# Performance work log

Hardware: AMD Instinct MI355X
Metric: run time of the kernel (lower is better)

## Reference

```python
import jax, jax.numpy as jnp
import numpy as np

B, J, V, G, D = 1, 24, 20000, 2, 3
DCIN = J * 12          # num_parts * (9 + 3)
DC = 4                 # d_cond
HID = 128
BETA = 100.0           # softplus beta
EPS = 1e-8


def softplus_b(x):
    return jax.nn.softplus(BETA * x) / BETA


def group_linear(x, W, b):
    # x: (J, N, din), W: (J, din, dout), b: (J, dout)
    return jnp.einsum('jnd,jdo->jno', x, W) + b[:, None, :]


def axis_angle_to_matrix(aa):
    # aa: (..., 3) -> (..., 3, 3), Rodrigues formula
    angle = jnp.linalg.norm(aa, axis=-1, keepdims=True)
    axis = aa / jnp.where(angle < 1e-12, 1.0, angle)
    x, y, z = axis[..., 0], axis[..., 1], axis[..., 2]
    a = angle[..., 0]
    c, s = jnp.cos(a), jnp.sin(a)
    C = 1.0 - c
    r0 = jnp.stack([c + x * x * C, x * y * C - z * s, x * z * C + y * s], axis=-1)
    r1 = jnp.stack([y * x * C + z * s, c + y * y * C, y * z * C - x * s], axis=-1)
    r2 = jnp.stack([z * x * C - y * s, z * y * C + x * s, c + z * z * C], axis=-1)
    return jnp.stack([r0, r1, r2], axis=-2)


def blending_weights(pts, Jtr_center, Jtr_neigh, Jtr_self, bid_this, bid_other, rigid_alpha, rigid_beta):
    # pts: (B,J,V,3); Jtr_*: (B,J,1,3); bid_*: (J,) int
    ra = jax.nn.elu(rigid_alpha - 1.0) + 1.0
    a_n = ra[bid_other, bid_this].reshape(1, -1, 1, 1)
    a_s = ra[bid_this, bid_other].reshape(1, -1, 1, 1)
    be_n = rigid_beta[bid_other, bid_this].reshape(1, -1, 1, 1)
    be_s = rigid_beta[bid_this, bid_other].reshape(1, -1, 1, 1)
    vec_bone_n = Jtr_neigh - Jtr_center
    vec_bone_s = Jtr_self - Jtr_center
    nb_n = jnp.linalg.norm(vec_bone_n, axis=-1, keepdims=True)
    nb_s = jnp.linalg.norm(vec_bone_s, axis=-1, keepdims=True)
    vb_n = (Jtr_neigh - Jtr_self) / (nb_n + nb_s + EPS) * nb_n
    vb_s = -vb_n / (nb_n + EPS) * nb_s
    n_n = jnp.linalg.norm(vb_n, axis=-1, keepdims=True)
    n_s = jnp.linalg.norm(vb_s, axis=-1, keepdims=True)
    tr_o = Jtr_neigh - vb_n
    vec_pts = jax.lax.stop_gradient(pts) - tr_o   # pts.detach() in torch
    d_n = vb_n / (n_n + EPS)
    d_s = vb_s / (n_s + EPS)
    r_n = jnp.sum(vec_pts * d_n, axis=-1, keepdims=True) / (n_n + EPS)
    r_s = jnp.sum(vec_pts * d_s, axis=-1, keepdims=True) / (n_s + EPS)
    return jax.nn.sigmoid((r_n * a_n + be_n) - (r_s * a_s + be_s))


def _forward(pts, Bcond, Btr, Brot, Bneigh, rigid_alpha, rigid_beta,
             cW0, cb0, cW1, cb1, cW2, cb2, W0, b0, W1, b1, W2, b2, W3, b3):
    # world -> per-part local coords: (B,J,V,3)
    Brot_inv = jnp.swapaxes(Brot, -1, -2)
    pts_local = jnp.einsum('bjxy,bjvy->bjvx', Brot_inv, pts[:, None] - Btr[:, :, None])
    # neighbor-based deformation offsets
    ids = jax.lax.stop_gradient(Bneigh[0, :, :, 4, :2]).astype(jnp.int32)  # (J,G,2)
    offset_sum = jnp.zeros_like(pts_local)
    for gi in range(G):  # small fixed neighbor count
        Jtr_this = Bneigh[:, :, gi, 0][:, :, None]    # (B,J,1,3)
        Jtr_center = Bneigh[:, :, gi, 1][:, :, None]
        Jtr_other = Bneigh[:, :, gi, 2][:, :, None]
        Jpose = Bneigh[:, :, gi, 3][:, :, None]
        w = blending_weights(pts_local, Jtr_center, Jtr_other, Jtr_this,
                             ids[:, gi, 0], ids[:, gi, 1], rigid_alpha, rigid_beta)  # (B,J,V,1)
        Jp_w = jnp.nan_to_num(Jpose * w)              # (B,J,V,3)
        R = axis_angle_to_matrix(-Jp_w)               # (B,J,V,3,3)
        off = jnp.einsum('bjvxy,bjvy->bjvx', R, pts_local - Jtr_center) + Jtr_center - pts_local
        offset_sum = offset_sum + jnp.nan_to_num(off)
    pts_local = pts_local + offset_sum
    # grouped per-part MLP (INR with num_groups=J)
    x_in = jnp.transpose(pts_local, (1, 0, 2, 3)).reshape(J, B * V, D)
    cond = jnp.broadcast_to(jnp.transpose(Bcond, (1, 0, 2))[:, :, None, :], (J, B, V, DCIN)).reshape(J, B * V, DCIN)
    c = softplus_b(group_linear(cond, cW0, cb0))
    c = softplus_b(group_linear(c, cW1, cb1))
    c = group_linear(c, cW2, cb2)                      # (J, BV, 4)
    x = jnp.concatenate([x_in, c], axis=-1)            # (J, BV, 7)
    x = softplus_b(group_linear(x, W0, b0))
    x = softplus_b(group_linear(x, W1, b1))
    x = softplus_b(group_linear(x, W2, b2))
    x = group_linear(x, W3, b3)                        # (J, BV, 1)
    pred_parts = jnp.transpose(x.reshape(J, B, V, 1), (1, 0, 2, 3))  # (B,J,V,1)
    # softmin blend over parts
    pred_min = jnp.min(pred_parts, axis=1)             # (B,V,1)
    delta = pred_parts - pred_min[:, None]
    wsm = jax.nn.softmax(-delta * 200.0, axis=1)       # Softmin(dim=1)
    return jnp.sum(delta * wsm, axis=1) + pred_min


def setup_inputs() -> dict:
    key = jax.random.key(0)
    ks = jax.random.split(key, 16)
    pts = jax.random.normal(ks[0], (B, V, D), jnp.float32)
    Bcond = jax.random.normal(ks[1], (B, J, DCIN), jnp.float32) * 0.1
    Btr = jax.random.normal(ks[2], (B, J, D), jnp.float32)
    Brot = jax.random.normal(ks[3], (B, J, D, D), jnp.float32)
    core = jax.random.normal(ks[4], (B, J, G, 4, D), jnp.float32) * 0.5
    ids_this = jnp.arange(J, dtype=jnp.float32)
    ids_o0 = jnp.mod(jnp.arange(J) + 1, J).astype(jnp.float32)
    ids_o1 = jnp.mod(jnp.arange(J) - 1, J).astype(jnp.float32)
    bid = jnp.zeros((B, J, G, 1, D), jnp.float32)
    bid = bid.at[:, :, 0, 0, 0].set(ids_this).at[:, :, 0, 0, 1].set(ids_o0)
    bid = bid.at[:, :, 1, 0, 0].set(ids_this).at[:, :, 1, 0, 1].set(ids_o1)
    Bneigh = jnp.concatenate([core, bid], axis=-2)     # (B,J,G,5,D)
    rigid_alpha = jnp.full((J, J), 2.0, jnp.float32)   # blend_alpha init
    rigid_beta = jnp.zeros((J, J), jnp.float32)
    def gl(k, din, dout, std):
        return jax.random.normal(k, (J, din, dout), jnp.float32) * std, jnp.zeros((J, dout), jnp.float32)
    cW0, cb0 = gl(ks[5], DCIN, DC * 4, float(np.sqrt(2.0 / DCIN)))
    cW1, cb1 = gl(ks[6], DC * 4, DC * 4, float(np.sqrt(2.0 / (DC * 4))))
    cW2, cb2 = gl(ks[7], DC * 4, DC, 1e-5)
    std_h = float(np.sqrt(2.0) / np.sqrt(HID))
    W0, b0 = gl(ks[8], D + DC, HID, std_h)
    W1, b1 = gl(ks[9], HID, HID, std_h)
    W2, b2 = gl(ks[10], HID, HID, std_h)
    W3 = jax.random.normal(ks[11], (J, HID, 1), jnp.float32) * 1e-5 + float(np.sqrt(np.pi) / np.sqrt(HID))
    b3 = jnp.full((J, 1), -1.0, jnp.float32)           # -radius_init
    return {'pts': pts, 'Bcond': Bcond, 'Btr': Btr, 'Brot': Brot, 'Bneigh': Bneigh,
            'rigid_alpha': rigid_alpha, 'rigid_beta': rigid_beta,
            'cW0': cW0, 'cb0': cb0, 'cW1': cW1, 'cb1': cb1, 'cW2': cW2, 'cb2': cb2,
            'W0': W0, 'b0': b0, 'W1': W1, 'b1': b1, 'W2': W2, 'b2': b2, 'W3': W3, 'b3': b3}


def reference(pts, Bcond, Btr, Brot, Bneigh, rigid_alpha, rigid_beta,
              cW0, cb0, cW1, cb1, cW2, cb2, W0, b0, W1, b1, W2, b2, W3, b3):
    return _forward(pts, Bcond, Btr, Brot, Bneigh, rigid_alpha, rigid_beta,
                    cW0, cb0, cW1, cb1, cW2, cb2, W0, b0, W1, b1, W2, b2, W3, b3)
```

## Files before the change

kernel.cpp:

```cpp
#include <hip/hip_runtime.h>
#include <hip/hip_bf16.h>
#include <math.h>

#define VN 20000
#define JN 24
#define TILE 64
#define KP 132
#define EPSF 1e-8f

typedef __attribute__((ext_vector_type(8))) short bfrag;
typedef __attribute__((ext_vector_type(4))) float f32x4;

#define WJ_STRIDE 139264
#define L0A 0
#define L0B 4096
#define L1A 8192
#define L1B 40960
#define L2A 73728
#define L2B 106496

__device__ __forceinline__ unsigned short f2bf(float x) {
    __hip_bfloat16 b = __float2bfloat16(x);
    unsigned short u; __builtin_memcpy(&u, &b, 2); return u;
}
__device__ __forceinline__ float bf2f(unsigned short u) {
    __hip_bfloat16 b; __builtin_memcpy(&b, &u, 2);
    return __bfloat162float(b);
}
__device__ __forceinline__ unsigned int pack_hl(float x) {
    const unsigned int h = (__float_as_uint(x) + 0x8000u) & 0xffff0000u;
    const float hf = __uint_as_float(h);
    const float lo = x - hf;
    unsigned int r;
    asm("v_cvt_pk_bf16_f32 %0, %1, %2" : "=v"(r) : "v"(hf), "v"(lo));
    return r;
}

__device__ __forceinline__ float softplus_fast(float x) {
    const float u = __builtin_amdgcn_exp2f(-144.269504f * fabsf(x));
    float p = fmaf(u, 3.04480e-4f, -1.31584e-3f);
    p = fmaf(u, p, 2.852768e-3f);
    p = fmaf(u, p, -4.902308e-3f);
    p = fmaf(u, p, 9.992342e-3f);
    p = fmaf(u, p, 8.0e-8f);
    return fmaxf(x, 0.0f) + p;
}

__global__ __launch_bounds__(384) void prep_kernel(
    const float* __restrict__ Bcond, const float* __restrict__ Bneigh,
    const float* __restrict__ ralpha, const float* __restrict__ rbeta,
    const float* __restrict__ cW0, const float* __restrict__ cb0,
    const float* __restrict__ cW1, const float* __restrict__ cb1,
    const float* __restrict__ cW2, const float* __restrict__ cb2,
    float* __restrict__ c4, float* __restrict__ geom)
{
    __shared__ float hbuf[JN][16];
    const int t = threadIdx.x;

    if (t < JN * 2) {
        const int j = t >> 1, gi = t & 1;
        const float* nb = Bneigh + (j * 2 + gi) * 15;
        const float tx = nb[0],  ty = nb[1],  tz = nb[2];
        const float cx = nb[3],  cy = nb[4],  cz = nb[5];
        const float ox = nb[6],  oy = nb[7],  oz = nb[8];
        const float px = nb[9],  py = nb[10], pz = nb[11];
        const int bid_this  = (int)nb[12];
        const int bid_other = (int)nb[13];
        const float xa_n = ralpha[bid_other * JN + bid_this] - 1.0f;
        const float xa_s = ralpha[bid_this * JN + bid_other] - 1.0f;
        const float a_n = xa_n > 0.0f ? xa_n + 1.0f : expf(xa_n);
        const float a_s = xa_s > 0.0f ? xa_s + 1.0f : expf(xa_s);
        const float be_n = rbeta[bid_other * JN + bid_this];
        const float be_s = rbeta[bid_this * JN + bid_other];

        const float bnx = ox - cx, bny = oy - cy, bnz = oz - cz;
        const float bsx = tx - cx, bsy = ty - cy, bsz = tz - cz;
        const float nb_n = sqrtf(bnx*bnx + bny*bny + bnz*bnz);
        const float nb_s = sqrtf(bsx*bsx + bsy*bsy + bsz*bsz);
        const float f = nb_n / (nb_n + nb_s + EPSF);
        const float vbnx = (ox - tx) * f, vbny = (oy - ty) * f, vbnz = (oz - tz) * f;
        const float g2 = -nb_s / (nb_n + EPSF);
        const float vbsx = vbnx * g2, vbsy = vbny * g2, vbsz = vbnz * g2;
        const float n_n = sqrtf(vbnx*vbnx + vbny*vbny + vbnz*vbnz);
        const float n_s = sqrtf(vbsx*vbsx + vbsy*vbsy + vbsz*vbsz);
        const float trx = ox - vbnx, tr_y = oy - vbny, trz = oz - vbnz;
        const float inn = 1.0f / ((n_n + EPSF) * (n_n + EPSF));
        const float ins = 1.0f / ((n_s + EPSF) * (n_s + EPSF));
        const float gx = vbnx * inn * a_n - vbsx * ins * a_s;
        const float gy = vbny * inn * a_n - vbsy * ins * a_s;
        const float gz = vbnz * inn * a_n - vbsz * ins * a_s;
        const float h = -(trx * gx + tr_y * gy + trz * gz) + be_n - be_s;
        float* gm = geom + (j * 2 + gi) * 12;
        gm[0] = gx; gm[1] = gy; gm[2] = gz; gm[3] = h;
        gm[4] = px; gm[5] = py; gm[6] = pz;
        gm[7] = cx; gm[8] = cy; gm[9] = cz;
        gm[10] = 0.0f; gm[11] = 0.0f;
    }

    {
        const int j = t >> 4, o = t & 15;
        const float* cond = Bcond + j * 288;
        const float* w = cW0 + j * 288 * 16 + o;
        float acc = cb0[j * 16 + o];
        for (int d = 0; d < 288; ++d) acc = fmaf(cond[d], w[d * 16], acc);
        hbuf[j][o] = softplus_fast(acc);
    }
    __syncthreads();
    {
        const int j = t >> 4, o = t & 15;
        const float* w = cW1 + j * 256 + o;
        float acc = cb1[j * 16 + o];
        #pragma unroll
        for (int d = 0; d < 16; ++d) acc = fmaf(hbuf[j][d], w[d * 16], acc);
        acc = softplus_fast(acc);
        __syncthreads();
        hbuf[j][o] = acc;
    }
    __syncthreads();
    if (t < JN * 4) {
        const int j = t >> 2, o = t & 3;
        const float* w = cW2 + j * 64 + o;
        float acc = cb2[j * 4 + o];
        #pragma unroll
        for (int d = 0; d < 16; ++d) acc = fmaf(hbuf[j][d], w[d * 4], acc);
        c4[j * 4 + o] = acc;
    }
}

__global__ __launch_bounds__(256) void wprep_kernel(
    const float* __restrict__ W0, const float* __restrict__ W1,
    const float* __restrict__ W2, unsigned short* __restrict__ wt)
{
    const int g = blockIdx.x * 256 + threadIdx.x;
    const int jj = g / 17408;
    const int r = (g - jj * 17408) * 8;
    const float* src; int kin, pr; bool loP;
    if (r < 8192)       { src = W0 + jj * 896;   kin = 7;   pr = r & 4095;          loP = r >= L0B; }
    else if (r < 73728) { src = W1 + jj * 16384; kin = 128; pr = (r - L1A) & 32767; loP = r >= L1B; }
    else                { src = W2 + jj * 16384; kin = 128; pr = (r - L2A) & 32767; loP = r >= L2B; }
    const int lane = (pr >> 3) & 63;
    const int nt   = (pr >> 9) & 7;
    const int ks   = pr >> 12;
    const int n  = nt * 16 + (lane & 15);
    const int k0 = (ks * 32 + (lane >> 4) * 8) >> 1;
    unsigned short out[8];
    #pragma unroll
    for (int kk = 0; kk < 4; ++kk) {
        const float v = (k0 + kk < kin) ? src[(k0 + kk) * 128 + n] : 0.0f;
        const unsigned short h = f2bf(v);
        if (!loP) { out[2*kk] = h; out[2*kk+1] = h; }
        else      { out[2*kk] = f2bf(v - bf2f(h)); out[2*kk+1] = 0; }
    }
    *(uint4*)(wt + jj * WJ_STRIDE + r) = *(const uint4*)out;
}

template<int NKS>
__device__ __forceinline__ void mfma_layer(
    unsigned int* __restrict__ X,
    const unsigned short* __restrict__ wA,
    const unsigned short* __restrict__ wB,
    const float* __restrict__ bvec,
    int q, int lane)
{
    const int l = lane & 15;
    const int quad = lane >> 4;
    const float bia0 = bvec[q * 32 + l];
    const float bia1 = bvec[q * 32 + 16 + l];
    f32x4 acc[4][2];
    #pragma unroll
    for (int mi = 0; mi < 4; ++mi) {
        acc[mi][0] = (f32x4){bia0, bia0, bia0, bia0};
        acc[mi][1] = (f32x4){bia1, bia1, bia1, bia1};
    }

    #pragma unroll 2
    for (int ks = 0; ks < NKS; ++ks) {
        bfrag bA[2], bB[2];
        #pragma unroll
        for (int ni = 0; ni < 2; ++ni) {
            const int off = ((ks * 8 + (q * 2 + ni)) * 64 + lane) * 8;
            bA[ni] = *(const bfrag*)(wA + off);
            bB[ni] = *(const bfrag*)(wB + off);
        }
        #pragma unroll
        for (int mi = 0; mi < 4; ++mi) {
            const bfrag a = *(const bfrag*)(
                (const unsigned short*)(X + (mi * 16 + l) * KP) + ks * 32 + quad * 8);
            #pragma unroll
            for (int ni = 0; ni < 2; ++ni) {
                acc[mi][ni] = __builtin_amdgcn_mfma_f32_16x16x32_bf16(a, bA[ni], acc[mi][ni], 0, 0, 0);
                acc[mi][ni] = __builtin_amdgcn_mfma_f32_16x16x32_bf16(a, bB[ni], acc[mi][ni], 0, 0, 0);
            }
        }
    }
    __syncthreads();
    #pragma unroll
    for (int ni = 0; ni < 2; ++ni) {
        const int ch = q * 32 + ni * 16 + l;
        #pragma unroll
        for (int mi = 0; mi < 4; ++mi) {
            #pragma unroll
            for (int r = 0; r < 4; ++r) {
                const float v = softplus_fast(acc[mi][ni][r]);
                const int p = mi * 16 + quad * 4 + r;
                X[p * KP + ch] = pack_hl(v);
            }
        }
    }
    __syncthreads();
}

__global__ __launch_bounds__(256, 4) void main_kernel(
    const float* __restrict__ pts, const float* __restrict__ Btr,
    const float* __restrict__ Brot,
    const float* __restrict__ b0, const float* __restrict__ b1,
    const float* __restrict__ b2, const float* __restrict__ W3,
    const float* __restrict__ b3,
    const float* __restrict__ c4, const float* __restrict__ geom,
    const unsigned short* __restrict__ wt,
    float* __restrict__ pred)
{
    __shared__ unsigned int X[TILE * KP];
    const int j = blockIdx.y;
    const int v0 = blockIdx.x * TILE;
    const int t = threadIdx.x;
    const int lane = t & 63;
    const int q = __builtin_amdgcn_readfirstlane(t >> 6);

    if (t < TILE) {
        const int v = v0 + t;
        float plx = 0.0f, ply = 0.0f, plz = 0.0f;
        if (v < VN) {
            const float dx = pts[v * 3 + 0] - Btr[j * 3 + 0];
            const float dy = pts[v * 3 + 1] - Btr[j * 3 + 1];
            const float dz = pts[v * 3 + 2] - Btr[j * 3 + 2];
            const float* R = Brot + j * 9;
            plx = R[0] * dx + R[3] * dy + R[6] * dz;
            ply = R[1] * dx + R[4] * dy + R[7] * dz;
            plz = R[2] * dx + R[5] * dy + R[8] * dz;
            float osx = 0.0f, osy = 0.0f, osz = 0.0f;
            #pragma unroll
            for (int gi = 0; gi < 2; ++gi) {
                const float* gm = geom + (j * 2 + gi) * 12;
                const float arg = plx * gm[0] + ply * gm[1] + plz * gm[2] + gm[3];
                const float w = 1.0f / (1.0f + __expf(-arg));
                const float aax = -gm[4] * w, aay = -gm[5] * w, aaz = -gm[6] * w;
                const float jcx = gm[7], jcy = gm[8], jcz = gm[9];
                const float ang = sqrtf(aax * aax + aay * aay + aaz * aaz);
                const float inv = ang < 1e-12f ? 1.0f : 1.0f / ang;
                const float ux = aax * inv, uy = aay * inv, uz = aaz * inv;
                const float co = __cosf(ang), si = __sinf(ang), C = 1.0f - co;
                const float vx = plx - jcx, vy = ply - jcy, vz = plz - jcz;
                const float du = ux * vx + uy * vy + uz * vz;
                const float cxv = uy * vz - uz * vy;
                const float cyv = uz * vx - ux * vz;
                const float czv = ux * vy - uy * vx;
                float offx = co * vx + si * cxv + C * ux * du + jcx - plx;
                float offy = co * vy + si * cyv + C * uy * du + jcy - ply;
                float offz = co * vz + si * czv + C * uz * du + jcz - plz;
                if (isnan(offx)) offx = 0.0f;
                if (isnan(offy)) offy = 0.0f;
                if (isnan(offz)) offz = 0.0f;
                osx += offx; osy += offy; osz += offz;
            }
            plx += osx; ply += osy; plz += osz;
        }
        X[t * KP + 0] = pack_hl(plx);
        X[t * KP + 1] = pack_hl(ply);
        X[t * KP + 2] = pack_hl(plz);
        X[t * KP + 3] = pack_hl(c4[j * 4 + 0]);
        X[t * KP + 4] = pack_hl(c4[j * 4 + 1]);
        X[t * KP + 5] = pack_hl(c4[j * 4 + 2]);
        X[t * KP + 6] = pack_hl(c4[j * 4 + 3]);
        #pragma unroll
        for (int k = 7; k < 16; ++k) X[t * KP + k] = 0u;
    }
    __syncthreads();

    const unsigned short* wj = wt + j * WJ_STRIDE;
    mfma_layer<1>(X, wj + L0A, wj + L0B, b0 + j * 128, q, lane);
    mfma_layer<8>(X, wj + L1A, wj + L1B, b1 + j * 128, q, lane);
    mfma_layer<8>(X, wj + L2A, wj + L2B, b2 + j * 128, q, lane);

    {
        const float* w3 = W3 + j * 128 + q * 32;
        float part = 0.0f;
        #pragma unroll 8
        for (int kk = 0; kk < 32; ++kk) {
            const unsigned int d = X[lane * KP + q * 32 + kk];
            const float xv = __uint_as_float(d << 16)
                           + __uint_as_float(d & 0xffff0000u);
            part = fmaf(xv, w3[kk], part);
        }
        X[lane * KP + 128 + q] = __float_as_uint(part);
    }
    __syncthreads();
    if (t < TILE) {
        const int v = v0 + t;
        const float r = b3[j]
            + __uint_as_float(X[t * KP + 128]) + __uint_as_float(X[t * KP + 129])
            + __uint_as_float(X[t * KP + 130]) + __uint_as_float(X[t * KP + 131]);
        if (v < VN) pred[j * VN + v] = r;
    }
}

__global__ __launch_bounds__(256) void softmin_kernel(const float* __restrict__ pred,
                                                      float* __restrict__ out)
{
    const int v = blockIdx.x * 256 + threadIdx.x;
    if (v >= VN) return;
    float vals[JN];
    float m = 3.4e38f;
    #pragma unroll
    for (int jj = 0; jj < JN; ++jj) {
        vals[jj] = pred[jj * VN + v];
        m = fminf(m, vals[jj]);
    }
    float s1 = 0.0f, s2 = 0.0f;
    #pragma unroll
    for (int jj = 0; jj < JN; ++jj) {
        const float d = vals[jj] - m;
        const float e = __expf(-200.0f * d);
        s1 += e;
        s2 = fmaf(d, e, s2);
    }
    out[v] = s2 / s1 + m;
}

extern "C" void kernel_launch(void* const* d_in, const int* in_sizes, int n_in,
                              void* d_out, int out_size, void* d_ws, size_t ws_size,
                              hipStream_t stream)
{
    const float* pts    = (const float*)d_in[0];
    const float* Bcond  = (const float*)d_in[1];
    const float* Btr    = (const float*)d_in[2];
    const float* Brot   = (const float*)d_in[3];
    const float* Bneigh = (const float*)d_in[4];
    const float* ralpha = (const float*)d_in[5];
    const float* rbeta  = (const float*)d_in[6];
    const float* cW0 = (const float*)d_in[7];
    const float* cb0 = (const float*)d_in[8];
    const float* cW1 = (const float*)d_in[9];
    const float* cb1 = (const float*)d_in[10];
    const float* cW2 = (const float*)d_in[11];
    const float* cb2 = (const float*)d_in[12];
    const float* W0 = (const float*)d_in[13];
    const float* b0 = (const float*)d_in[14];
    const float* W1 = (const float*)d_in[15];
    const float* b1 = (const float*)d_in[16];
    const float* W2 = (const float*)d_in[17];
    const float* b2 = (const float*)d_in[18];
    const float* W3 = (const float*)d_in[19];
    const float* b3 = (const float*)d_in[20];

    float* ws   = (float*)d_ws;
    float* pred = ws;
    float* c4   = ws + JN * VN;
    float* geom = c4 + JN * 4;
    unsigned short* wt = (unsigned short*)(geom + JN * 2 * 12);

    prep_kernel<<<1, 384, 0, stream>>>(Bcond, Bneigh, ralpha, rbeta,
                                       cW0, cb0, cW1, cb1, cW2, cb2, c4, geom);

    wprep_kernel<<<(JN * 17408) / 256, 256, 0, stream>>>(W0, W1, W2, wt);

    dim3 grid((VN + TILE - 1) / TILE, JN);
    main_kernel<<<grid, 256, 0, stream>>>(pts, Btr, Brot,
                                          b0, b1, b2, W3, b3,
                                          c4, geom, wt, pred);

    softmin_kernel<<<(VN + 255) / 256, 256, 0, stream>>>(pred, (float*)d_out);
}
```

Measured before the change: 262.2 us.

## Merge prep kernels and remap main grid so each XCD owns three parts

```diff
diff --git a/kernel.cpp b/kernel.cpp
--- a/kernel.cpp
+++ b/kernel.cpp
@@ -7,6 +7,8 @@
 #define TILE 64
 #define KP 132
 #define EPSF 1e-8f
+#define NXB 313
+#define WPREP_BLOCKS 1632
 
 typedef __attribute__((ext_vector_type(8))) short bfrag;
 typedef __attribute__((ext_vector_type(4))) float f32x4;
@@ -46,7 +48,9 @@
     return fmaxf(x, 0.0f) + p;
 }
 
-__global__ __launch_bounds__(384) void prep_kernel(
+__global__ __launch_bounds__(256) void setup_kernel(
+    const float* __restrict__ W0, const float* __restrict__ W1,
+    const float* __restrict__ W2, unsigned short* __restrict__ wt,
     const float* __restrict__ Bcond, const float* __restrict__ Bneigh,
     const float* __restrict__ ralpha, const float* __restrict__ rbeta,
     const float* __restrict__ cW0, const float* __restrict__ cb0,
@@ -54,11 +58,41 @@
     const float* __restrict__ cW2, const float* __restrict__ cb2,
     float* __restrict__ c4, float* __restrict__ geom)
 {
-    __shared__ float hbuf[JN][16];
+    if (blockIdx.x < WPREP_BLOCKS) {
+        const int g = blockIdx.x * 256 + threadIdx.x;
+        const int jj = g / 17408;
+        const int r = (g - jj * 17408) * 8;
+        const float* src; int kin, pr; bool loP;
+        if (r < 8192)       { src = W0 + jj * 896;   kin = 7;   pr = r & 4095;          loP = r >= L0B; }
+        else if (r < 73728) { src = W1 + jj * 16384; kin = 128; pr = (r - L1A) & 32767; loP = r >= L1B; }
+        else                { src = W2 + jj * 16384; kin = 128; pr = (r - L2A) & 32767; loP = r >= L2B; }
+        const int lane = (pr >> 3) & 63;
+        const int nt   = (pr >> 9) & 7;
+        const int ks   = pr >> 12;
+        const int n  = nt * 16 + (lane & 15);
+        const int k0 = (ks * 32 + (lane >> 4) * 8) >> 1;
+        unsigned short out[8];
+        #pragma unroll
+        for (int kk = 0; kk < 4; ++kk) {
+            const float v = (k0 + kk < kin) ? src[(k0 + kk) * 128 + n] : 0.0f;
+            const unsigned short h = f2bf(v);
+            if (!loP) { out[2*kk] = h; out[2*kk+1] = h; }
+            else      { out[2*kk] = f2bf(v - bf2f(h)); out[2*kk+1] = 0; }
+        }
+        *(uint4*)(wt + jj * WJ_STRIDE + r) = *(const uint4*)out;
+        return;
+    }
+
+    __shared__ float cond_s[288];
+    __shared__ float sh[16][17];
+    __shared__ float hb[16];
+    const int j = blockIdx.x - WPREP_BLOCKS;
     const int t = threadIdx.x;
 
-    if (t < JN * 2) {
-        const int j = t >> 1, gi = t & 1;
+    for (int i = t; i < 288; i += 256) cond_s[i] = Bcond[j * 288 + i];
+
+    if (t < 2) {
+        const int gi = t;
         const float* nb = Bneigh + (j * 2 + gi) * 15;
         const float tx = nb[0],  ty = nb[1],  tz = nb[2];
         const float cx = nb[3],  cy = nb[4],  cz = nb[5];
@@ -96,62 +130,40 @@
         gm[7] = cx; gm[8] = cy; gm[9] = cz;
         gm[10] = 0.0f; gm[11] = 0.0f;
     }
+    __syncthreads();
 
     {
-        const int j = t >> 4, o = t & 15;
-        const float* cond = Bcond + j * 288;
+        const int o = t & 15, c = t >> 4;
         const float* w = cW0 + j * 288 * 16 + o;
-        float acc = cb0[j * 16 + o];
-        for (int d = 0; d < 288; ++d) acc = fmaf(cond[d], w[d * 16], acc);
-        hbuf[j][o] = softplus_fast(acc);
-    }
-    __syncthreads();
-    {
-        const int j = t >> 4, o = t & 15;
-        const float* w = cW1 + j * 256 + o;
-        float acc = cb1[j * 16 + o];
-        #pragma unroll
-        for (int d = 0; d < 16; ++d) acc = fmaf(hbuf[j][d], w[d * 16], acc);
-        acc = softplus_fast(acc);
-        __syncthreads();
-        hbuf[j][o] = acc;
-    }
-    __syncthreads();
-    if (t < JN * 4) {
-        const int j = t >> 2, o = t & 3;
-        const float* w = cW2 + j * 64 + o;
-        float acc = cb2[j * 4 + o];
-        #pragma unroll
-        for (int d = 0; d < 16; ++d) acc = fmaf(hbuf[j][d], w[d * 4], acc);
-        c4[j * 4 + o] = acc;
-    }
-}
-
-__global__ __launch_bounds__(256) void wprep_kernel(
-    const float* __restrict__ W0, const float* __restrict__ W1,
-    const float* __restrict__ W2, unsigned short* __restrict__ wt)
-{
-    const int g = blockIdx.x * 256 + threadIdx.x;
-    const int jj = g / 17408;
-    const int r = (g - jj * 17408) * 8;
-    const float* src; int kin, pr; bool loP;
-    if (r < 8192)       { src = W0 + jj * 896;   kin = 7;   pr = r & 4095;          loP = r >= L0B; }
-    else if (r < 73728) { src = W1 + jj * 16384; kin = 128; pr = (r - L1A) & 32767; loP = r >= L1B; }
-    else                { src = W2 + jj * 16384; kin = 128; pr = (r - L2A) & 32767; loP = r >= L2B; }
-    const int lane = (pr >> 3) & 63;
-    const int nt   = (pr >> 9) & 7;
-    const int ks   = pr >> 12;
-    const int n  = nt * 16 + (lane & 15);
-    const int k0 = (ks * 32 + (lane >> 4) * 8) >> 1;
-    unsigned short out[8];
-    #pragma unroll
-    for (int kk = 0; kk < 4; ++kk) {
-        const float v = (k0 + kk < kin) ? src[(k0 + kk) * 128 + n] : 0.0f;
-        const unsigned short h = f2bf(v);
-        if (!loP) { out[2*kk] = h; out[2*kk+1] = h; }
-        else      { out[2*kk] = f2bf(v - bf2f(h)); out[2*kk+1] = 0; }
-    }
-    *(uint4*)(wt + jj * WJ_STRIDE + r) = *(const uint4*)out;
+        const int d0 = c * 18;
+        float acc = 0.0f;
+        #pragma unroll
+        for (int d = 0; d < 18; ++d) acc = fmaf(cond_s[d0 + d], w[(d0 + d) * 16], acc);
+        sh[c][o] = acc;
+    }
+    __syncthreads();
+    if (t < 16) {
+        float acc = cb0[j * 16 + t];
+        #pragma unroll
+        for (int c = 0; c < 16; ++c) acc += sh[c][t];
+        hb[t] = softplus_fast(acc);
+    }
+    __syncthreads();
+    if (t < 16) {
+        const float* w = cW1 + j * 256 + t;
+        float acc = cb1[j * 16 + t];
+        #pragma unroll
+        for (int d = 0; d < 16; ++d) acc = fmaf(hb[d], w[d * 16], acc);
+        sh[0][t] = softplus_fast(acc);
+    }
+    __syncthreads();
+    if (t < 4) {
+        const float* w = cW2 + j * 64 + t;
+        float acc = cb2[j * 4 + t];
+        #pragma unroll
+        for (int d = 0; d < 16; ++d) acc = fmaf(sh[0][d], w[d * 4], acc);
+        c4[j * 4 + t] = acc;
+    }
 }
 
 template<int NKS>
@@ -221,8 +233,11 @@
     float* __restrict__ pred)
 {
     __shared__ unsigned int X[TILE * KP];
-    const int j = blockIdx.y;
-    const int v0 = blockIdx.x * TILE;
+    const int bid = blockIdx.x;
+    const int xcd = bid & 7;
+    const int s = bid >> 3;
+    const int j = xcd * 3 + (s % 3);
+    const int v0 = (s / 3) * TILE;
     const int t = threadIdx.x;
     const int lane = t & 63;
     const int q = __builtin_amdgcn_readfirstlane(t >> 6);
@@ -359,15 +374,14 @@
     float* geom = c4 + JN * 4;
     unsigned short* wt = (unsigned short*)(geom + JN * 2 * 12);
 
-    prep_kernel<<<1, 384, 0, stream>>>(Bcond, Bneigh, ralpha, rbeta,
-                                       cW0, cb0, cW1, cb1, cW2, cb2, c4, geom);
-
-    wprep_kernel<<<(JN * 17408) / 256, 256, 0, stream>>>(W0, W1, W2, wt);
-
-    dim3 grid((VN + TILE - 1) / TILE, JN);
-    main_kernel<<<grid, 256, 0, stream>>>(pts, Btr, Brot,
-                                          b0, b1, b2, W3, b3,
-                                          c4, geom, wt, pred);
+    setup_kernel<<<WPREP_BLOCKS + JN, 256, 0, stream>>>(
+        W0, W1, W2, wt,
+        Bcond, Bneigh, ralpha, rbeta,
+        cW0, cb0, cW1, cb1, cW2, cb2, c4, geom);
+
+    main_kernel<<<8 * 3 * NXB, 256, 0, stream>>>(pts, Btr, Brot,
+                                                 b0, b1, b2, W3, b3,
+                                                 c4, geom, wt, pred);
 
     softmin_kernel<<<(VN + 255) / 256, 256, 0, stream>>>(pred, (float*)d_out);
 }
```

Result: no change. 257.8 us (-1.7%).
